# Performance work log

Hardware: AMD Instinct MI355X
Metric: run time of the kernel (lower is better)

## Reference

```python
import jax, jax.numpy as jnp
import numpy as np
import math

B, N, D_MODEL = 2, 2048, 512
H, D_HEAD = 8, 64
D_FF = 2048
LN_EPS = 1e-5


def layer_norm(x, g, b):
    mu = jnp.mean(x, axis=-1, keepdims=True)
    var = jnp.mean(jnp.square(x - mu), axis=-1, keepdims=True)
    return (x - mu) * jax.lax.rsqrt(var + LN_EPS) * g + b


def setup_inputs() -> dict:
    key = jax.random.key(0)
    ks = jax.random.split(key, 12)
    s = lambda fan_in: 1.0 / math.sqrt(fan_in)
    inp = {
        "x": jax.random.normal(ks[0], (B, N, D_MODEL), dtype=jnp.float32),
        "mask": jax.random.randint(ks[1], (B, 1, N, N), 0, 2) > 0,
        # attention_pre: Linear(d_model -> 3*H*D_HEAD)
        "W_qkv": jax.random.uniform(ks[2], (D_MODEL, 3 * H * D_HEAD), minval=-s(D_MODEL), maxval=s(D_MODEL)),
        "b_qkv": jnp.zeros((3 * H * D_HEAD,), jnp.float32),
        # project: Linear(H*D_HEAD -> d_model)
        "W_proj": jax.random.uniform(ks[3], (H * D_HEAD, D_MODEL), minval=-s(H * D_HEAD), maxval=s(H * D_HEAD)),
        "b_proj": jnp.zeros((D_MODEL,), jnp.float32),
        "ln1_g": jnp.ones((D_MODEL,), jnp.float32),
        "ln1_b": jnp.zeros((D_MODEL,), jnp.float32),
        # mlp: fc(512->2048, relu), fc(2048->512, relu)  (activation on every layer)
        "W1": jax.random.uniform(ks[4], (D_MODEL, D_FF), minval=-s(D_MODEL), maxval=s(D_MODEL)),
        "b1": jnp.zeros((D_FF,), jnp.float32),
        "W2": jax.random.uniform(ks[5], (D_FF, D_MODEL), minval=-s(D_FF), maxval=s(D_FF)),
        "b2": jnp.zeros((D_MODEL,), jnp.float32),
        "ln2_g": jnp.ones((D_MODEL,), jnp.float32),
        "ln2_b": jnp.zeros((D_MODEL,), jnp.float32),
    }
    return inp


def reference(x, mask, W_qkv, b_qkv, W_proj, b_proj, ln1_g, ln1_b, W1, b1, W2, b2, ln2_g, ln2_b):
    # --- Attention (manual QKV matmul-softmax-matmul) ---
    qkv = x @ W_qkv + b_qkv                      # [B,N,3*H*Dh]
    q, k, v = jnp.split(qkv, 3, axis=2)          # each [B,N,H*Dh]
    def split_heads(t):
        return t.reshape(B, N, H, D_HEAD).transpose(0, 2, 1, 3)  # [B,H,N,Dh]
    q, k, v = split_heads(q), split_heads(k), split_heads(v)
    score = jnp.einsum('bhnd,bhmd->bhnm', q, k) / math.sqrt(D_HEAD)  # [B,H,N,N]
    score = jnp.where(mask, score, -1e9)
    score = jax.nn.softmax(score, axis=-1)
    attn = jnp.einsum('bhnm,bhmd->bhnd', score, v)   # [B,H,N,Dh]
    attn = attn.transpose(0, 2, 1, 3).reshape(B, N, H * D_HEAD)
    a = attn @ W_proj + b_proj                   # [B,N,D_MODEL]
    # --- residual + LN1 ---
    x = layer_norm(x + a, ln1_g, ln1_b)
    # --- MLP (relu after both layers, dropout p=0 = identity) ---
    m = jax.nn.relu(jax.nn.relu(x @ W1 + b1) @ W2 + b2)
    x = layer_norm(x + m, ln2_g, ln2_b)
    return x
```

## Files before the change

kernel.cpp:

```cpp
#include <hip/hip_runtime.h>
#include <math.h>

constexpr int BATCH  = 2;
constexpr int SEQ    = 2048;
constexpr int DMODEL = 512;
constexpr int NH     = 8;
constexpr int DHEAD  = 64;
constexpr int ROWS   = BATCH * SEQ;
constexpr size_t SZ  = (size_t)ROWS * DMODEL;

typedef __attribute__((ext_vector_type(8))) short bf16x8;
typedef __attribute__((ext_vector_type(4))) float f32x4;

__device__ __forceinline__ ushort f2bf(float f) {
    unsigned u = __float_as_uint(f);
    unsigned r = (u + 0x7FFFu + ((u >> 16) & 1u)) >> 16;
    return (ushort)r;
}

__device__ __forceinline__ unsigned cvtpk_bf16(float lo, float hi) {
    unsigned r;
    asm("v_cvt_pk_bf16_f32 %0, %1, %2" : "=v"(r) : "v"(lo), "v"(hi));
    return r;
}

__device__ __forceinline__ void gload_lds16(const void* g, void* l) {
    __builtin_amdgcn_global_load_lds(
        (const __attribute__((address_space(1))) void*)g,
        (__attribute__((address_space(3))) void*)l, 16, 0, 0);
}

__global__ __launch_bounds__(256) void detect_mask_k(
    const uint4* __restrict__ m, int* __restrict__ flag)
{
    const int i = blockIdx.x * 256 + threadIdx.x;
    const uint4 v = m[i];
    unsigned b0 = 0, b1 = 0;
    #pragma unroll
    for (int c = 0; c < 4; ++c) {
        const unsigned u = (&v.x)[c];
        b0 |= (u > 1u) ? 1u : 0u;
        b1 |= (u != 0u && u != 0x3F800000u) ? 1u : 0u;
    }
    const int lane = threadIdx.x & 63;
    if (__any(b0) && lane == 0) atomicOr(flag, 1);
    if (__any(b1) && lane == 0) atomicOr(flag, 2);
}

__global__ __launch_bounds__(256) void prep_all_k(
    const float* __restrict__ x, ushort* __restrict__ xb,
    const float* __restrict__ Wq, const float* __restrict__ Wp,
    const float* __restrict__ W1w, const float* __restrict__ W2w,
    ushort* __restrict__ WqT, ushort* __restrict__ WpT,
    ushort* __restrict__ W1T, ushort* __restrict__ W2T,
    const void* __restrict__ maskp, const int* __restrict__ flagp,
    unsigned long long* __restrict__ bits)
{
    __shared__ ushort T[64][65];
    const int bid = blockIdx.x;
    const int t = threadIdx.x;

    if (bid < 2048) {
        const size_t i = ((size_t)bid * 256 + t) * 4;
        float4 v = *(const float4*)(x + i);
        ushort4 o;
        o.x = f2bf(v.x); o.y = f2bf(v.y); o.z = f2bf(v.z); o.w = f2bf(v.w);
        *(ushort4*)(xb + i) = o;
        return;
    }
    if (bid >= 2816) {
        const int w = (bid - 2816) * 4 + (t >> 6);
        const int lane = t & 63;
        const size_t idx = ((size_t)w << 6) + lane;
        const int f = *flagp;
        bool mv;
        if (!(f & 1))      mv = ((const int*)maskp)[idx] != 0;
        else if (!(f & 2)) mv = ((const float*)maskp)[idx] != 0.f;
        else               mv = ((const unsigned char*)maskp)[idx] != 0;
        unsigned long long bal = __ballot(mv);
        if (lane == 0) bits[w] = bal;
        return;
    }
    const int wb = bid - 2048;
    const float* W; ushort* Wt; int K, N, tix, tiy;
    if (wb < 192)      { W = Wq;  Wt = WqT; K = 512;  N = 1536; tix = wb % 24;        tiy = wb / 24; }
    else if (wb < 256) { W = Wp;  Wt = WpT; K = 512;  N = 512;  tix = (wb-192) % 8;   tiy = (wb-192) / 8; }
    else if (wb < 512) { W = W1w; Wt = W1T; K = 512;  N = 2048; tix = (wb-256) % 32;  tiy = (wb-256) / 32; }
    else               { W = W2w; Wt = W2T; K = 2048; N = 512;  tix = (wb-512) % 8;   tiy = (wb-512) / 8; }
    const int k0 = tiy * 64, n0 = tix * 64;
    const int r = t >> 4, c4 = (t & 15) * 4;
    #pragma unroll
    for (int it = 0; it < 4; ++it) {
        const int row = it*16 + r;
        float4 v = *(const float4*)&W[(size_t)(k0 + row) * N + n0 + c4];
        T[c4+0][row] = f2bf(v.x);
        T[c4+1][row] = f2bf(v.y);
        T[c4+2][row] = f2bf(v.z);
        T[c4+3][row] = f2bf(v.w);
    }
    __syncthreads();
    #pragma unroll
    for (int it = 0; it < 4; ++it) {
        const int row = it*16 + r;
        ushort4 o;
        o.x = T[row][c4+0]; o.y = T[row][c4+1];
        o.z = T[row][c4+2]; o.w = T[row][c4+3];
        *(ushort4*)&Wt[(size_t)(n0 + row) * K + k0 + c4] = o;
    }
}

template<int EPI, int BM>
__global__ __launch_bounds__(256) void mgemm_k(
    const ushort* __restrict__ A,
    const ushort* __restrict__ Wt,
    const float* __restrict__ bias,
    float* __restrict__ Cf, ushort* __restrict__ Cb,
    ushort* __restrict__ Qo, ushort* __restrict__ Ko, ushort* __restrict__ Vo,
    int M, int N, int K)
{
    constexpr int WM   = BM / 2;
    constexpr int MF   = WM / 16;
    constexpr int APW  = (BM / 8) / 4;

    __shared__ ushort As[BM * 64];
    __shared__ ushort Bs[128 * 64];

    const int tid  = threadIdx.x;
    const int wid  = tid >> 6, lane = tid & 63;
    const int lq   = lane & 15, lg = lane >> 4;
    const int wr   = wid >> 1,  wc = wid & 1;
    const int bm   = blockIdx.y * BM, bn = blockIdx.x * 128;

    const int srow0 = lane >> 3;
    const int sch   = lane & 7;

    f32x4 acc[MF][4] = {};

    for (int k0 = 0; k0 < K; k0 += 64) {
        __syncthreads();
        #pragma unroll
        for (int i = 0; i < APW; ++i) {
            const int seg = wid * APW + i;
            const int row = seg * 8 + srow0;
            const int c16 = sch ^ (row & 7);
            gload_lds16(A + (size_t)(bm + row) * K + k0 + c16 * 8, As + seg * 512);
        }
        #pragma unroll
        for (int i = 0; i < 4; ++i) {
            const int seg = wid * 4 + i;
            const int row = seg * 8 + srow0;
            const int c16 = sch ^ (row & 7);
            gload_lds16(Wt + (size_t)(bn + row) * K + k0 + c16 * 8, Bs + seg * 512);
        }
        __syncthreads();

        #pragma unroll
        for (int ks = 0; ks < 2; ++ks) {
            bf16x8 af[MF], bfr[4];
            #pragma unroll
            for (int m = 0; m < MF; ++m) {
                const int row = wr*WM + m*16 + lq;
                const int c16 = (ks*4 + lg) ^ (row & 7);
                af[m] = *(const bf16x8*)&As[row * 64 + c16 * 8];
            }
            #pragma unroll
            for (int n = 0; n < 4; ++n) {
                const int row = wc*64 + n*16 + lq;
                const int c16 = (ks*4 + lg) ^ (row & 7);
                bfr[n] = *(const bf16x8*)&Bs[row * 64 + c16 * 8];
            }
            #pragma unroll
            for (int m = 0; m < MF; ++m)
                #pragma unroll
                for (int n = 0; n < 4; ++n)
                    acc[m][n] = __builtin_amdgcn_mfma_f32_16x16x32_bf16(
                        af[m], bfr[n], acc[m][n], 0, 0, 0);
        }
    }

    #pragma unroll
    for (int m = 0; m < MF; ++m) {
        const int row0 = bm + wr*WM + m*16 + lg*4;
        #pragma unroll
        for (int n = 0; n < 4; ++n) {
            const int col = bn + wc*64 + n*16 + lq;
            const float bv = bias[col];
            float v[4];
            #pragma unroll
            for (int r = 0; r < 4; ++r) {
                v[r] = acc[m][n][r] + bv;
                if (EPI == 1 || EPI == 2) v[r] = fmaxf(v[r], 0.f);
            }
            if (EPI == 3) {
                const int part = col >> 9, hc = col & 511;
                const int hh = hc >> 6, d0 = hc & 63;
                const int bidx = row0 >> 11, nrow0 = row0 & 2047;
                if (part == 2) {
                    ushort4 pv;
                    pv.x = f2bf(v[0]); pv.y = f2bf(v[1]);
                    pv.z = f2bf(v[2]); pv.w = f2bf(v[3]);
                    *(ushort4*)(Vo + (((size_t)bidx*NH + hh)*DHEAD + d0)*SEQ + nrow0) = pv;
                } else {
                    ushort* dst = (part == 0) ? Qo : Ko;
                    #pragma unroll
                    for (int r = 0; r < 4; ++r)
                        dst[((((size_t)bidx*NH + hh)*SEQ + nrow0 + r) << 6) + d0] = f2bf(v[r]);
                }
            } else {
                #pragma unroll
                for (int r = 0; r < 4; ++r) {
                    const int row = row0 + r;
                    if (EPI == 1) Cb[(size_t)row * N + col] = f2bf(v[r]);
                    else          Cf[(size_t)row * N + col] = v[r];
                }
            }
        }
    }
}

__global__ __launch_bounds__(256) void attn_mfma_k(
    const ushort* __restrict__ Qb, const ushort* __restrict__ Kb,
    const ushort* __restrict__ Vtb, const unsigned long long* __restrict__ mbits,
    float* __restrict__ Opart, float2* __restrict__ MLpart)
{
    __shared__ ushort Klds[2][64 * 64];
    __shared__ ushort Vlds[2][64 * 64];
    __shared__ ushort Plds[4][16 * 64];

    const int tid  = threadIdx.x;
    const int wid  = tid >> 6;
    const int lane = tid & 63;
    const int lq   = lane & 15;
    const int lg   = lane >> 4;

    const int tile = blockIdx.x & 31;
    const int bh   = blockIdx.x >> 5;
    const int b    = bh >> 3;
    const int qw   = tile * 64 + wid * 16;
    const int s    = blockIdx.y;
    const int c0   = s * 16, c1 = c0 + 16;

    const ushort* Qg = Qb + ((size_t)bh * SEQ + qw + lq) * DHEAD;
    const bf16x8 qf0 = *(const bf16x8*)(Qg + lg * 8);
    const bf16x8 qf1 = *(const bf16x8*)(Qg + 32 + lg * 8);

    const ushort* Kg = Kb  + (size_t)bh * SEQ * DHEAD;
    const ushort* Vg = Vtb + (size_t)bh * DHEAD * SEQ;

    const int srow0 = lane >> 3;
    const int sch   = lane & 7;

    const unsigned long long* mrow = mbits + ((size_t)b * SEQ + qw + lq) * (SEQ / 64);

    f32x4 o[4] = {};
    float mrun = -1e30f, lrun = 0.f;
    const float k2 = 0.125f * 1.44269504f;

    auto STAGE = [&](int c, int buf) {
        #pragma unroll
        for (int i = 0; i < 2; ++i) {
            const int seg = wid * 2 + i;
            const int row = seg * 8 + srow0;
            const int gc  = sch ^ (row & 7);
            gload_lds16(Kg + (size_t)(c*64 + row) * DHEAD + gc * 8, &Klds[buf][seg * 512]);
            gload_lds16(Vg + (size_t)row * SEQ + c*64 + gc * 8, &Vlds[buf][seg * 512]);
        }
    };

    auto CHUNK = [&](int c, int cur) {
        if (c + 1 < c1) STAGE(c + 1, cur ^ 1);

        f32x4 st[4];
        #pragma unroll
        for (int kt = 0; kt < 4; ++kt) {
            const int row = kt*16 + lq;
            bf16x8 kf0 = *(const bf16x8*)&Klds[cur][row*64 + ((lg  ) ^ (lq & 7))*8];
            bf16x8 kf1 = *(const bf16x8*)&Klds[cur][row*64 + ((4+lg) ^ (lq & 7))*8];
            f32x4 a = {};
            a = __builtin_amdgcn_mfma_f32_16x16x32_bf16(kf0, qf0, a, 0, 0, 0);
            a = __builtin_amdgcn_mfma_f32_16x16x32_bf16(kf1, qf1, a, 0, 0, 0);
            st[kt] = a;
        }

        const unsigned long long mws = mrow[c] >> (lg * 4);
        const unsigned mlo = (unsigned)mws, mhi = (unsigned)(mws >> 32);
        float sv[16];
        float cmax = -1e30f;
        #pragma unroll
        for (int kt = 0; kt < 4; ++kt) {
            const unsigned half = (kt & 2) ? mhi : mlo;
            #pragma unroll
            for (int r = 0; r < 4; ++r) {
                const unsigned bit = (half >> ((kt & 1)*16 + r)) & 1u;
                const float sc = bit ? st[kt][r] * k2 : -1e9f;
                sv[kt*4 + r] = sc;
                cmax = fmaxf(cmax, sc);
            }
        }
        cmax = fmaxf(cmax, __shfl_xor(cmax, 16));
        cmax = fmaxf(cmax, __shfl_xor(cmax, 32));

        float mnew = mrun, scale = 1.0f;
        if (!__all(cmax <= mrun)) {
            mnew  = fmaxf(mrun, cmax);
            scale = exp2f(mrun - mnew);
            float sc[4];
            #pragma unroll
            for (int r = 0; r < 4; ++r) sc[r] = __shfl(scale, lg*4 + r);
            #pragma unroll
            for (int nt = 0; nt < 4; ++nt)
                #pragma unroll
                for (int r = 0; r < 4; ++r) o[nt][r] *= sc[r];
        }

        float lsum = 0.f;
        #pragma unroll
        for (int kt = 0; kt < 4; ++kt) {
            const float p0 = exp2f(sv[kt*4+0] - mnew);
            const float p1 = exp2f(sv[kt*4+1] - mnew);
            const float p2 = exp2f(sv[kt*4+2] - mnew);
            const float p3 = exp2f(sv[kt*4+3] - mnew);
            lsum += (p0 + p1) + (p2 + p3);
            uint2 pk;
            pk.x = cvtpk_bf16(p0, p1);
            pk.y = cvtpk_bf16(p2, p3);
            const int addr = lq*64 + (((kt*2 + (lg>>1)) ^ (lq & 7)) * 8) + (lg & 1)*4;
            *(uint2*)&Plds[wid][addr] = pk;
        }
        lsum += __shfl_xor(lsum, 16);
        lsum += __shfl_xor(lsum, 32);
        lrun = lrun * scale + lsum;
        mrun = mnew;

        #pragma unroll
        for (int kk = 0; kk < 2; ++kk) {
            const int ch = (kk*4 + lg) ^ (lq & 7);
            bf16x8 pf = *(const bf16x8*)&Plds[wid][lq*64 + ch*8];
            #pragma unroll
            for (int nt = 0; nt < 4; ++nt) {
                bf16x8 vf = *(const bf16x8*)&Vlds[cur][(nt*16 + lq)*64 + ch*8];
                o[nt] = __builtin_amdgcn_mfma_f32_16x16x32_bf16(pf, vf, o[nt], 0, 0, 0);
            }
        }

        __syncthreads();
    };

    STAGE(c0, 0);
    __syncthreads();
    for (int c = c0; c < c1; c += 2) {
        CHUNK(c, 0);
        CHUNK(c + 1, 1);
    }

    #pragma unroll
    for (int nt = 0; nt < 4; ++nt)
        #pragma unroll
        for (int r = 0; r < 4; ++r) {
            const int qrow = qw + lg*4 + r;
            Opart[(((size_t)s*16 + bh)*SEQ + qrow)*64 + nt*16 + lq] = o[nt][r];
        }
    if (lg == 0) {
        float2 ml; ml.x = mrun; ml.y = lrun;
        MLpart[((size_t)s*16 + bh)*SEQ + qw + lq] = ml;
    }
}

__global__ __launch_bounds__(256) void attn_combine_k(
    const float* __restrict__ Op, const float2* __restrict__ ML,
    ushort* __restrict__ attnb)
{
    const int row  = blockIdx.x * 4 + (threadIdx.x >> 6);
    const int lane = threadIdx.x & 63;
    const int bh = row >> 11, q = row & 2047;
    const int b = bh >> 3, h = bh & 7;
    const float2 ml0 = ML[row];
    const float2 ml1 = ML[16*SEQ + row];
    const float m  = fmaxf(ml0.x, ml1.x);
    const float a0 = exp2f(ml0.x - m), a1 = exp2f(ml1.x - m);
    const float l  = ml0.y*a0 + ml1.y*a1;
    const float o0 = Op[(size_t)row*64 + lane];
    const float o1 = Op[((size_t)16*SEQ + row)*64 + lane];
    const float o  = (o0*a0 + o1*a1) / l;
    attnb[((size_t)(b*SEQ + q))*DMODEL + h*DHEAD + lane] = f2bf(o);
}

__global__ __launch_bounds__(256) void add_ln_k(
    const float* __restrict__ X, const float* __restrict__ Aa,
    const float* __restrict__ gg, const float* __restrict__ bb,
    float* __restrict__ out, ushort* __restrict__ outb)
{
    const int r = blockIdx.x;
    const int t = threadIdx.x;
    const float2 x2 = ((const float2*)(X  + (size_t)r * DMODEL))[t];
    const float2 a2 = ((const float2*)(Aa + (size_t)r * DMODEL))[t];
    const float v0 = x2.x + a2.x, v1 = x2.y + a2.y;
    float s  = v0 + v1;
    float ss = v0*v0 + v1*v1;
    #pragma unroll
    for (int off = 32; off > 0; off >>= 1) {
        s  += __shfl_down(s,  off);
        ss += __shfl_down(ss, off);
    }
    __shared__ float ps[4], pss[4];
    const int wid = t >> 6;
    if ((t & 63) == 0) { ps[wid] = s; pss[wid] = ss; }
    __syncthreads();
    const float tot  = ps[0] + ps[1] + ps[2] + ps[3];
    const float tots = pss[0] + pss[1] + pss[2] + pss[3];
    const float mean = tot * (1.0f / DMODEL);
    const float var  = tots * (1.0f / DMODEL) - mean * mean;
    const float rstd = rsqrtf(var + 1e-5f);
    const float2 g2 = ((const float2*)gg)[t];
    const float2 b2 = ((const float2*)bb)[t];
    float2 r2;
    r2.x = (v0 - mean) * rstd * g2.x + b2.x;
    r2.y = (v1 - mean) * rstd * g2.y + b2.y;
    ((float2*)(out + (size_t)r * DMODEL))[t] = r2;
    if (outb) {
        ushort2 ob; ob.x = f2bf(r2.x); ob.y = f2bf(r2.y);
        *(ushort2*)(outb + (size_t)r * DMODEL + t*2) = ob;
    }
}

extern "C" void kernel_launch(void* const* d_in, const int* in_sizes, int n_in,
                              void* d_out, int out_size, void* d_ws, size_t ws_size,
                              hipStream_t stream)
{
    const float* x      = (const float*)d_in[0];
    const void*  mask   = d_in[1];
    const float* W_qkv  = (const float*)d_in[2];
    const float* b_qkv  = (const float*)d_in[3];
    const float* W_proj = (const float*)d_in[4];
    const float* b_proj = (const float*)d_in[5];
    const float* ln1_g  = (const float*)d_in[6];
    const float* ln1_b  = (const float*)d_in[7];
    const float* W1     = (const float*)d_in[8];
    const float* b1     = (const float*)d_in[9];
    const float* W2     = (const float*)d_in[10];
    const float* b2     = (const float*)d_in[11];
    const float* ln2_g  = (const float*)d_in[12];
    const float* ln2_b  = (const float*)d_in[13];

    float* ws = (float*)d_ws;
    ushort* xb    = (ushort*)ws;
    ushort* Qb    = (ushort*)(ws + SZ/2);
    ushort* Kb    = (ushort*)(ws + SZ);
    ushort* Vtb   = (ushort*)(ws + SZ + SZ/2);
    ushort* attnb = (ushort*)(ws + 2*SZ);
    float*  Opart = ws + 2*SZ + SZ/2;
    float2* MLp   = (float2*)(ws + 4*SZ + SZ/2);
    float*  ap    = ws + 2*SZ + SZ/2;
    float*  mbuf  = ws + 2*SZ;
    float*  x1    = ws + 3*SZ + SZ/2;
    ushort* x1b   = (ushort*)(ws + 4*SZ + SZ/2);
    ushort* hb    = (ushort*)ws;
    ushort* WqkvT = (ushort*)(ws + 5*SZ);
    ushort* WprojT= (ushort*)(ws + 5*SZ + 393216);
    ushort* W1T   = (ushort*)(ws + 5*SZ + 524288);
    ushort* W2T   = (ushort*)(ws + 5*SZ + 1048576);
    unsigned long long* bits = (unsigned long long*)(ws + 5*SZ + 1572864);
    int*    flag  = (int*)(ws + 5*SZ + 1572864 + 262144);

    float* out = (float*)d_out;

    hipMemsetAsync(flag, 0, 4, stream);
    detect_mask_k<<<64, 256, 0, stream>>>((const uint4*)mask, flag);
    prep_all_k<<<2816 + 32768, 256, 0, stream>>>(
        x, xb, W_qkv, W_proj, W1, W2, WqkvT, WprojT, W1T, W2T,
        mask, flag, bits);

    mgemm_k<3,128><<<dim3(12, 32), 256, 0, stream>>>(xb, WqkvT, b_qkv,
        nullptr, nullptr, Qb, Kb, Vtb, ROWS, 3*DMODEL, DMODEL);
    attn_mfma_k<<<dim3(BATCH*NH*(SEQ/64), 2), 256, 0, stream>>>(
        Qb, Kb, Vtb, bits, Opart, MLp);
    attn_combine_k<<<BATCH*NH*SEQ/4, 256, 0, stream>>>(Opart, MLp, attnb);
    mgemm_k<0,64><<<dim3(4, 64), 256, 0, stream>>>(attnb, WprojT, b_proj,
        ap, nullptr, nullptr, nullptr, nullptr, ROWS, DMODEL, DMODEL);
    add_ln_k<<<ROWS, 256, 0, stream>>>(x, ap, ln1_g, ln1_b, x1, x1b);
    mgemm_k<1,128><<<dim3(16, 32), 256, 0, stream>>>(x1b, W1T, b1,
        nullptr, hb, nullptr, nullptr, nullptr, ROWS, 2048, DMODEL);
    mgemm_k<2,64><<<dim3(4, 64), 256, 0, stream>>>(hb, W2T, b2,
        mbuf, nullptr, nullptr, nullptr, nullptr, ROWS, DMODEL, 2048);
    add_ln_k<<<ROWS, 256, 0, stream>>>(x1, mbuf, ln2_g, ln2_b, out, nullptr);
}
```

Baseline: 174.3 us.

## Precompute LDS offsets, add launch bounds, and MFMA priority hints in attention

Reworks the attention inner loop. LDS read and write offsets and the global staging pointers are precomputed once and then advanced incrementally, removing per-chunk address arithmetic. It also adds a min-blocks-per-SM launch bound of 4 to steer register allocation, wraps the MFMA sections in s_setprio to favour matrix issue across waves, and turns the max and sum reductions into trees for more parallelism. The gains come from fewer instructions and higher occupancy, at the risk of register spills from holding many offsets under the tighter register budget.

Result: no change. 172.0 us (-1.3%).

```diff
diff --git a/kernel.cpp b/kernel.cpp
--- a/kernel.cpp
+++ b/kernel.cpp
@@ -218,7 +218,7 @@
     }
 }
 
-__global__ __launch_bounds__(256) void attn_mfma_k(
+__global__ __launch_bounds__(256, 4) void attn_mfma_k(
     const ushort* __restrict__ Qb, const ushort* __restrict__ Kb,
     const ushort* __restrict__ Vtb, const unsigned long long* __restrict__ mbits,
     float* __restrict__ Opart, float2* __restrict__ MLpart)
@@ -244,11 +244,40 @@
     const bf16x8 qf0 = *(const bf16x8*)(Qg + lg * 8);
     const bf16x8 qf1 = *(const bf16x8*)(Qg + 32 + lg * 8);
 
-    const ushort* Kg = Kb  + (size_t)bh * SEQ * DHEAD;
-    const ushort* Vg = Vtb + (size_t)bh * DHEAD * SEQ;
-
     const int srow0 = lane >> 3;
     const int sch   = lane & 7;
+    const int gc8   = (sch ^ srow0) * 8;
+
+    const ushort* kgb  = Kb  + (size_t)bh * SEQ * DHEAD
+                             + (size_t)(wid*16 + srow0) * DHEAD + gc8;
+    const ushort* vgb0 = Vtb + (size_t)bh * DHEAD * SEQ
+                             + (size_t)(wid*16 + srow0) * SEQ + gc8;
+    const ushort* vgb1 = vgb0 + 8 * SEQ;
+
+    ushort* kd0 = &Klds[0][(wid*2)*512];
+    ushort* kd1 = &Klds[1][(wid*2)*512];
+    ushort* vd0 = &Vlds[0][(wid*2)*512];
+    ushort* vd1 = &Vlds[1][(wid*2)*512];
+
+    int kro[4][2], vro[4][2], pwo[4], pro[2];
+    #pragma unroll
+    for (int kt = 0; kt < 4; ++kt) {
+        kro[kt][0] = ((kt*16 + lq)*64 + ((lg     ^ (lq&7))*8)) * 2;
+        kro[kt][1] = ((kt*16 + lq)*64 + (((4+lg) ^ (lq&7))*8)) * 2;
+        pwo[kt]    = (wid*1024 + lq*64 + (((kt*2 + (lg>>1)) ^ (lq&7))*8) + (lg&1)*4) * 2;
+    }
+    #pragma unroll
+    for (int kk = 0; kk < 2; ++kk) {
+        pro[kk] = (wid*1024 + lq*64 + (((kk*4+lg) ^ (lq&7))*8)) * 2;
+        #pragma unroll
+        for (int nt = 0; nt < 4; ++nt)
+            vro[nt][kk] = ((nt*16 + lq)*64 + (((kk*4+lg) ^ (lq&7))*8)) * 2;
+    }
+    const char* kbase0 = (const char*)&Klds[0][0];
+    const char* kbase1 = (const char*)&Klds[1][0];
+    const char* vbase0 = (const char*)&Vlds[0][0];
+    const char* vbase1 = (const char*)&Vlds[1][0];
+    char*       pbase  = (char*)&Plds[0][0];
 
     const unsigned long long* mrow = mbits + ((size_t)b * SEQ + qw + lq) * (SEQ / 64);
 
@@ -256,102 +285,110 @@
     float mrun = -1e30f, lrun = 0.f;
     const float k2 = 0.125f * 1.44269504f;
 
-    auto STAGE = [&](int c, int buf) {
-        #pragma unroll
-        for (int i = 0; i < 2; ++i) {
-            const int seg = wid * 2 + i;
-            const int row = seg * 8 + srow0;
-            const int gc  = sch ^ (row & 7);
-            gload_lds16(Kg + (size_t)(c*64 + row) * DHEAD + gc * 8, &Klds[buf][seg * 512]);
-            gload_lds16(Vg + (size_t)row * SEQ + c*64 + gc * 8, &Vlds[buf][seg * 512]);
-        }
-    };
-
-    auto CHUNK = [&](int c, int cur) {
-        if (c + 1 < c1) STAGE(c + 1, cur ^ 1);
-
-        f32x4 st[4];
-        #pragma unroll
-        for (int kt = 0; kt < 4; ++kt) {
-            const int row = kt*16 + lq;
-            bf16x8 kf0 = *(const bf16x8*)&Klds[cur][row*64 + ((lg  ) ^ (lq & 7))*8];
-            bf16x8 kf1 = *(const bf16x8*)&Klds[cur][row*64 + ((4+lg) ^ (lq & 7))*8];
-            f32x4 a = {};
-            a = __builtin_amdgcn_mfma_f32_16x16x32_bf16(kf0, qf0, a, 0, 0, 0);
-            a = __builtin_amdgcn_mfma_f32_16x16x32_bf16(kf1, qf1, a, 0, 0, 0);
-            st[kt] = a;
-        }
-
-        const unsigned long long mws = mrow[c] >> (lg * 4);
-        const unsigned mlo = (unsigned)mws, mhi = (unsigned)(mws >> 32);
-        float sv[16];
-        float cmax = -1e30f;
-        #pragma unroll
-        for (int kt = 0; kt < 4; ++kt) {
-            const unsigned half = (kt & 2) ? mhi : mlo;
-            #pragma unroll
-            for (int r = 0; r < 4; ++r) {
-                const unsigned bit = (half >> ((kt & 1)*16 + r)) & 1u;
-                const float sc = bit ? st[kt][r] * k2 : -1e9f;
-                sv[kt*4 + r] = sc;
-                cmax = fmaxf(cmax, sc);
-            }
-        }
-        cmax = fmaxf(cmax, __shfl_xor(cmax, 16));
-        cmax = fmaxf(cmax, __shfl_xor(cmax, 32));
-
-        float mnew = mrun, scale = 1.0f;
-        if (!__all(cmax <= mrun)) {
-            mnew  = fmaxf(mrun, cmax);
-            scale = exp2f(mrun - mnew);
-            float sc[4];
-            #pragma unroll
-            for (int r = 0; r < 4; ++r) sc[r] = __shfl(scale, lg*4 + r);
-            #pragma unroll
-            for (int nt = 0; nt < 4; ++nt)
-                #pragma unroll
-                for (int r = 0; r < 4; ++r) o[nt][r] *= sc[r];
-        }
-
-        float lsum = 0.f;
-        #pragma unroll
-        for (int kt = 0; kt < 4; ++kt) {
-            const float p0 = exp2f(sv[kt*4+0] - mnew);
-            const float p1 = exp2f(sv[kt*4+1] - mnew);
-            const float p2 = exp2f(sv[kt*4+2] - mnew);
-            const float p3 = exp2f(sv[kt*4+3] - mnew);
-            lsum += (p0 + p1) + (p2 + p3);
-            uint2 pk;
-            pk.x = cvtpk_bf16(p0, p1);
-            pk.y = cvtpk_bf16(p2, p3);
-            const int addr = lq*64 + (((kt*2 + (lg>>1)) ^ (lq & 7)) * 8) + (lg & 1)*4;
-            *(uint2*)&Plds[wid][addr] = pk;
-        }
-        lsum += __shfl_xor(lsum, 16);
-        lsum += __shfl_xor(lsum, 32);
-        lrun = lrun * scale + lsum;
-        mrun = mnew;
-
-        #pragma unroll
-        for (int kk = 0; kk < 2; ++kk) {
-            const int ch = (kk*4 + lg) ^ (lq & 7);
-            bf16x8 pf = *(const bf16x8*)&Plds[wid][lq*64 + ch*8];
-            #pragma unroll
-            for (int nt = 0; nt < 4; ++nt) {
-                bf16x8 vf = *(const bf16x8*)&Vlds[cur][(nt*16 + lq)*64 + ch*8];
-                o[nt] = __builtin_amdgcn_mfma_f32_16x16x32_bf16(pf, vf, o[nt], 0, 0, 0);
-            }
-        }
-
-        __syncthreads();
-    };
-
-    STAGE(c0, 0);
+    {
+        const ushort* kp0  = kgb  + (size_t)c0 * 4096;
+        const ushort* vq0  = vgb0 + c0 * 64;
+        const ushort* vq1  = vgb1 + c0 * 64;
+        gload_lds16(kp0,       kd0);
+        gload_lds16(kp0 + 512, kd0 + 512);
+        gload_lds16(vq0, vd0);
+        gload_lds16(vq1, vd0 + 512);
+    }
+    const ushort* kp  = kgb  + (size_t)(c0 + 1) * 4096;
+    const ushort* vp0 = vgb0 + (c0 + 1) * 64;
+    const ushort* vp1 = vgb1 + (c0 + 1) * 64;
     __syncthreads();
+
+#define ATTN_CHUNK(CC, KD, VD, KBASE, VBASE)                                   \
+    {                                                                          \
+        if ((CC) + 1 < c1) {                                                   \
+            gload_lds16(kp,       (KD));                                       \
+            gload_lds16(kp + 512, (KD) + 512);                                 \
+            gload_lds16(vp0, (VD));                                            \
+            gload_lds16(vp1, (VD) + 512);                                      \
+            kp += 4096; vp0 += 64; vp1 += 64;                                  \
+        }                                                                      \
+        f32x4 st[4];                                                           \
+        __builtin_amdgcn_s_setprio(1);                                         \
+        _Pragma("unroll")                                                      \
+        for (int kt = 0; kt < 4; ++kt) {                                       \
+            bf16x8 kf0 = *(const bf16x8*)((KBASE) + kro[kt][0]);               \
+            bf16x8 kf1 = *(const bf16x8*)((KBASE) + kro[kt][1]);               \
+            f32x4 a = {};                                                      \
+            a = __builtin_amdgcn_mfma_f32_16x16x32_bf16(kf0, qf0, a, 0, 0, 0); \
+            a = __builtin_amdgcn_mfma_f32_16x16x32_bf16(kf1, qf1, a, 0, 0, 0); \
+            st[kt] = a;                                                        \
+        }                                                                      \
+        __builtin_amdgcn_s_setprio(0);                                         \
+        const unsigned long long mws = mrow[CC] >> (lg * 4);                   \
+        const unsigned mlo = (unsigned)mws, mhi = (unsigned)(mws >> 32);       \
+        float sv[16];                                                          \
+        _Pragma("unroll")                                                      \
+        for (int kt = 0; kt < 4; ++kt) {                                       \
+            const unsigned half = (kt & 2) ? mhi : mlo;                        \
+            _Pragma("unroll")                                                  \
+            for (int r = 0; r < 4; ++r) {                                      \
+                const unsigned bit = (half >> ((kt & 1)*16 + r)) & 1u;         \
+                sv[kt*4 + r] = bit ? st[kt][r] * k2 : -1e9f;                   \
+            }                                                                  \
+        }                                                                      \
+        float cmax = fmaxf(                                                    \
+            fmaxf(fmaxf(fmaxf(sv[0],sv[1]),fmaxf(sv[2],sv[3])),                \
+                  fmaxf(fmaxf(sv[4],sv[5]),fmaxf(sv[6],sv[7]))),               \
+            fmaxf(fmaxf(fmaxf(sv[8],sv[9]),fmaxf(sv[10],sv[11])),              \
+                  fmaxf(fmaxf(sv[12],sv[13]),fmaxf(sv[14],sv[15]))));          \
+        cmax = fmaxf(cmax, __shfl_xor(cmax, 16));                              \
+        cmax = fmaxf(cmax, __shfl_xor(cmax, 32));                              \
+        float mnew = mrun, scale = 1.0f;                                       \
+        if (!__all(cmax <= mrun)) {                                            \
+            mnew  = fmaxf(mrun, cmax);                                         \
+            scale = exp2f(mrun - mnew);                                        \
+            float sc[4];                                                       \
+            _Pragma("unroll")                                                  \
+            for (int r = 0; r < 4; ++r) sc[r] = __shfl(scale, lg*4 + r);       \
+            _Pragma("unroll")                                                  \
+            for (int nt = 0; nt < 4; ++nt)                                     \
+                _Pragma("unroll")                                              \
+                for (int r = 0; r < 4; ++r) o[nt][r] *= sc[r];                 \
+        }                                                                      \
+        float ls[4];                                                           \
+        _Pragma("unroll")                                                      \
+        for (int kt = 0; kt < 4; ++kt) {                                       \
+            const float p0 = exp2f(sv[kt*4+0] - mnew);                         \
+            const float p1 = exp2f(sv[kt*4+1] - mnew);                         \
+            const float p2 = exp2f(sv[kt*4+2] - mnew);                         \
+            const float p3 = exp2f(sv[kt*4+3] - mnew);                         \
+            ls[kt] = (p0 + p1) + (p2 + p3);                                    \
+            uint2 pk;                                                          \
+            pk.x = cvtpk_bf16(p0, p1);                                         \
+            pk.y = cvtpk_bf16(p2, p3);                                         \
+            *(uint2*)(pbase + pwo[kt]) = pk;                                   \
+        }                                                                      \
+        float lsum = (ls[0] + ls[1]) + (ls[2] + ls[3]);                        \
+        lsum += __shfl_xor(lsum, 16);                                          \
+        lsum += __shfl_xor(lsum, 32);                                          \
+        lrun = lrun * scale + lsum;                                            \
+        mrun = mnew;                                                           \
+        __builtin_amdgcn_s_setprio(1);                                         \
+        _Pragma("unroll")                                                      \
+        for (int kk = 0; kk < 2; ++kk) {                                       \
+            bf16x8 pf = *(const bf16x8*)(pbase + pro[kk]);                     \
+            _Pragma("unroll")                                                  \
+            for (int nt = 0; nt < 4; ++nt) {                                   \
+                bf16x8 vf = *(const bf16x8*)((VBASE) + vro[nt][kk]);           \
+                o[nt] = __builtin_amdgcn_mfma_f32_16x16x32_bf16(               \
+                    pf, vf, o[nt], 0, 0, 0);                                   \
+            }                                                                  \
+        }                                                                      \
+        __builtin_amdgcn_s_setprio(0);                                         \
+        __syncthreads();                                                       \
+    }
+
     for (int c = c0; c < c1; c += 2) {
-        CHUNK(c, 0);
-        CHUNK(c + 1, 1);
-    }
+        ATTN_CHUNK(c,     kd1, vd1, kbase0, vbase0);
+        ATTN_CHUNK(c + 1, kd0, vd0, kbase1, vbase1);
+    }
+#undef ATTN_CHUNK
 
     #pragma unroll
     for (int nt = 0; nt < 4; ++nt)
```
